# Performance work log

Hardware: AMD Instinct MI355X
Metric: run time of the kernel (lower is better)

The kernel has to match this reference:

```python
import jax, jax.numpy as jnp
import numpy as np

B, S, H, NH, HD = 2, 2048, 2048, 16, 128


def _bit_linear(x, w):
    """Ternary STE BitLinear: absmean scaling, round/clamp, fp matmul, rescale."""
    eps = 1e-5
    wn = w / (jnp.abs(w).mean() + eps)
    # straight-through estimator: forward uses quantized weights, grad flows to wn
    wq = wn + jax.lax.stop_gradient(jnp.clip(jnp.round(wn), -1.0, 1.0) - wn)
    y = x @ wq.T
    scale = w.shape[1]  # in_features
    Qb = 128.0  # 2**(8-1)
    return jnp.clip(y / scale * Qb, -Qb, Qb)


def _rotate_half(x):
    x1, x2 = jnp.split(x, 2, axis=-1)
    return jnp.concatenate([-x2, x1], axis=-1)


def setup_inputs() -> dict:
    key = jax.random.key(0)
    k1, k2, k3 = jax.random.split(key, 3)
    x = jax.random.normal(k1, (B, S, H), dtype=jnp.float32)
    w_qkv = jax.random.normal(k2, (3 * H, H), dtype=jnp.float32) * 0.02
    w_o = jax.random.normal(k3, (H, H), dtype=jnp.float32) * 0.02
    # realistic RoPE table [2, S, HD]
    inv_freq = 1.0 / (10000.0 ** (jnp.arange(0, HD, 2, dtype=jnp.float32) / HD))
    freqs = jnp.arange(S, dtype=jnp.float32)[:, None] * inv_freq[None, :]
    emb = jnp.concatenate([freqs, freqs], axis=-1)  # [S, HD]
    rotary = jnp.stack([jnp.cos(emb), jnp.sin(emb)], axis=0)
    return {"x": x, "rotary": rotary, "w_qkv": w_qkv, "w_o": w_o}


def reference(x, rotary, w_qkv, w_o):
    qkv = _bit_linear(x, w_qkv)  # [B, S, 3H]
    q, k, v = jnp.split(qkv, 3, axis=-1)
    q = q.reshape(B, S, NH, HD)
    k = k.reshape(B, S, NH, HD)
    v = v.reshape(B, S, NH, HD)
    cos = rotary[0][None, :, None, :]  # [1, S, 1, HD]
    sin = rotary[1][None, :, None, :]
    q = q * cos + _rotate_half(q) * sin
    k = k * cos + _rotate_half(k) * sin
    # [B, NH, S, HD]
    q, k, v = (t.transpose(0, 2, 1, 3) for t in (q, k, v))
    scores = jnp.einsum("bhqd,bhkd->bhqk", q, k) / np.sqrt(HD).astype(np.float32)
    causal = jnp.tril(jnp.ones((S, S), dtype=bool))
    scores = jnp.where(causal[None, None], scores, -jnp.inf)
    attn = jax.nn.softmax(scores, axis=-1)
    y = jnp.einsum("bhqk,bhkd->bhqd", attn, v)
    y = y.transpose(0, 2, 1, 3).reshape(B, S, H)
    return _bit_linear(y, w_o)
```

## Files before the change

### kernel.cpp

```cpp
#include <hip/hip_runtime.h>
#include <hip/hip_bf16.h>
#include <stdint.h>

#define B_   2
#define S_   2048
#define H_   2048
#define NH_  16
#define HD_  128
#define MTOK 4096
#define NQKV 6144

typedef unsigned short u16;
typedef __attribute__((ext_vector_type(8))) __bf16 bf16x8;
typedef __attribute__((ext_vector_type(4))) float f32x4;
typedef __attribute__((ext_vector_type(16))) float f32x16;

static __device__ __forceinline__ float bf2f(u16 u){
  union { uint32_t i; float f; } v; v.i = ((uint32_t)u) << 16; return v.f;
}
static __device__ __forceinline__ u16 f2bf(float f){
  union { float f; uint32_t i; } v; v.f = f;
  uint32_t r = v.i + 0x7FFFu + ((v.i >> 16) & 1u);
  return (u16)(r >> 16);
}
static __device__ __forceinline__ uint32_t cvt_pk_bf16(float lo, float hi){
  uint32_t r;
  asm("v_cvt_pk_bf16_f32 %0, %1, %2" : "=v"(r) : "v"(lo), "v"(hi));
  return r;
}
static __device__ __forceinline__ void pl32swap(uint32_t &a, uint32_t &b){
  asm volatile("v_permlane32_swap_b32 %0, %1" : "+v"(a), "+v"(b));
}

__device__ __forceinline__ void gload_lds16(const void* g, void* l){
  __builtin_amdgcn_global_load_lds((const __attribute__((address_space(1))) void*)g,
                                   (__attribute__((address_space(3))) void*)l, 16, 0, 0);
}

__global__ void absum_kernel(const float* __restrict__ w, int n, float* __restrict__ partial){
  __shared__ float sm[256];
  float s = 0.f;
  for (int i = blockIdx.x*256 + threadIdx.x; i < n; i += gridDim.x*256)
    s += fabsf(w[i]);
  sm[threadIdx.x] = s; __syncthreads();
  for (int st = 128; st > 0; st >>= 1){
    if ((int)threadIdx.x < st) sm[threadIdx.x] += sm[threadIdx.x + st];
    __syncthreads();
  }
  if (threadIdx.x == 0) partial[blockIdx.x] = sm[0];
}

__global__ void finalize_kernel(const float* __restrict__ p1, const float* __restrict__ p2,
                                float* __restrict__ scales){
  __shared__ double sm[256];
  int t = threadIdx.x;
  double s = (double)p1[t] + (double)p1[t+256] + (double)p1[t+512] + (double)p1[t+768];
  sm[t] = s; __syncthreads();
  for (int st = 128; st > 0; st >>= 1){ if (t < st) sm[t] += sm[t+st]; __syncthreads(); }
  if (t == 0) scales[0] = (float)(1.0 / (sm[0] / (double)(3*H_*H_) + 1e-5));
  __syncthreads();
  s = (double)p2[t] + (double)p2[t+256] + (double)p2[t+512] + (double)p2[t+768];
  sm[t] = s; __syncthreads();
  for (int st = 128; st > 0; st >>= 1){ if (t < st) sm[t] += sm[t+st]; __syncthreads(); }
  if (t == 0) scales[1] = (float)(1.0 / (sm[0] / (double)(H_*H_) + 1e-5));
}

__global__ void quant_kernel(const float* __restrict__ w, u16* __restrict__ wq, int n,
                             const float* __restrict__ scales, int which){
  float inv = scales[which];
  for (int i = blockIdx.x*256 + threadIdx.x; i < n; i += gridDim.x*256){
    float q = rintf(w[i] * inv);
    q = fminf(1.f, fmaxf(-1.f, q));
    wq[i] = f2bf(q);
  }
}

__global__ void castx_kernel(const float* __restrict__ x, u16* __restrict__ xb, int n){
  int i = blockIdx.x*256 + threadIdx.x;
  if (i < n) xb[i] = f2bf(x[i]);
}

template<int EPI>
__global__ __launch_bounds__(256) void gemm_kernel(const u16* __restrict__ A,
    const u16* __restrict__ Bw, int M, int N, int K,
    float* __restrict__ outf, u16* __restrict__ qb, u16* __restrict__ kb, u16* __restrict__ vtb)
{
  __shared__ u16 As[128*32];
  __shared__ u16 Bs[128*32];
  int nbn = N >> 7;
  int nb_tot = (M >> 7) * nbn;
  int bid = blockIdx.x;
  int chunk = nb_tot >> 3;
  bid = (bid & 7) * chunk + (bid >> 3);
  int bm = bid / nbn, bn = bid % nbn;
  int m0 = bm << 7, n0 = bn << 7;
  int tid = threadIdx.x;
  int lane = tid & 63, wid = tid >> 6;
  int wr = wid >> 1, wc = wid & 1;
  int lg = lane >> 4, lr = lane & 15;

  const u16* Ab = A + m0 * K;
  const u16* Bb = Bw + n0 * K;
  int srow = tid >> 2;
  int scol = (tid & 3) << 3;

  f32x4 acc[4][4];
  #pragma unroll
  for (int i = 0; i < 4; i++)
    #pragma unroll
    for (int j = 0; j < 4; j++) acc[i][j] = f32x4{0.f,0.f,0.f,0.f};

  for (int k0 = 0; k0 < K; k0 += 32){
    gload_lds16(Ab + srow*K      + k0 + scol, As + tid*8);
    gload_lds16(Ab + (srow+64)*K + k0 + scol, As + 2048 + tid*8);
    gload_lds16(Bb + srow*K      + k0 + scol, Bs + tid*8);
    gload_lds16(Bb + (srow+64)*K + k0 + scol, Bs + 2048 + tid*8);
    __syncthreads();
    bf16x8 af[4], bfr[4];
    #pragma unroll
    for (int mi = 0; mi < 4; mi++) af[mi]  = *(const bf16x8*)(As + ((wr*64 + mi*16 + lr)*32 + lg*8));
    #pragma unroll
    for (int ni = 0; ni < 4; ni++) bfr[ni] = *(const bf16x8*)(Bs + ((wc*64 + ni*16 + lr)*32 + lg*8));
    #pragma unroll
    for (int mi = 0; mi < 4; mi++)
      #pragma unroll
      for (int ni = 0; ni < 4; ni++)
        acc[mi][ni] = __builtin_amdgcn_mfma_f32_16x16x32_bf16(af[mi], bfr[ni], acc[mi][ni], 0, 0, 0);
    __syncthreads();
  }

  #pragma unroll
  for (int mi = 0; mi < 4; mi++){
    #pragma unroll
    for (int ni = 0; ni < 4; ni++){
      int ncol = n0 + wc*64 + ni*16 + lr;
      #pragma unroll
      for (int r = 0; r < 4; r++){
        int m = m0 + wr*64 + mi*16 + lg*4 + r;
        float v = acc[mi][ni][r] * 0.0625f;
        v = fminf(128.f, fmaxf(-128.f, v));
        if (EPI == 1){
          outf[m*N + ncol] = v;
        } else {
          int b = m >> 11, s = m & 2047;
          int part = ncol >> 11, c = ncol & 2047;
          int h = c >> 7, d = c & 127;
          int bh = b*NH_ + h;
          u16 bv = f2bf(v);
          if (part == 0)      qb[((bh*S_ + s) << 7) + d] = bv;
          else if (part == 1) kb[((bh*S_ + s) << 7) + d] = bv;
          else                vtb[((bh*HD_ + d) << 11) + s] = bv;
        }
      }
    }
  }
}

__global__ void rope_kernel(u16* __restrict__ qb, u16* __restrict__ kb, const float* __restrict__ rot){
  int i = blockIdx.x*256 + threadIdx.x;
  int d = i & 63;
  int s = (i >> 6) & 2047;
  int bh = (i >> 17) & 31;
  u16* buf = (i >> 22) ? kb : qb;
  int base = (bh*S_ + s)*HD_;
  float c  = rot[s*HD_ + d];
  float sn = rot[S_*HD_ + s*HD_ + d];
  float x1 = bf2f(buf[base + d]);
  float x2 = bf2f(buf[base + d + 64]);
  buf[base + d]      = f2bf(x1*c - x2*sn);
  buf[base + d + 64] = f2bf(x2*c + x1*sn);
}

__global__ __launch_bounds__(256) void attn_kernel(const u16* __restrict__ qb,
    const u16* __restrict__ kb, const u16* __restrict__ vtb, u16* __restrict__ ao)
{
  __shared__ alignas(16) u16 Ks[2][4096];
  __shared__ alignas(16) u16 Vs[2][4096];

  int bid = blockIdx.x;
  int sbid = (bid & 7)*64 + (bid >> 3);
  int bh = sbid >> 4;
  int bq = 15 - (sbid & 15);
  int tid = threadIdx.x;
  int wid = tid >> 6, lane = tid & 63;
  int l31 = lane & 31, hl = lane >> 5;
  int q0 = bq * 128;
  int qw = q0 + wid*32;
  int q  = qw + l31;

  const u16* Qp = qb + (size_t)(bh*S_ + qw)*HD_;
  const u16* Kp = kb + (size_t)bh*S_*HD_;
  const u16* Vt = vtb + (size_t)bh*HD_*S_;

  bf16x8 qf[8];
  #pragma unroll
  for (int t = 0; t < 8; t++)
    qf[t] = *(const bf16x8*)(Qp + l31*HD_ + t*16 + hl*8);

  f32x16 o[4];
  #pragma unroll
  for (int i = 0; i < 4; i++)
    #pragma unroll
    for (int j = 0; j < 16; j++) o[i][j] = 0.f;
  float m_r = -1e30f, l_r = 0.f;
  const float sm_scale = 0.08838834764831845f;

  auto STAGE = [&](int buf, int kt2){
    int t0 = wid*2;
    gload_lds16(Kp + (size_t)(kt2 + l31)*HD_ + (t0  )*16 + hl*8, &Ks[buf][((t0  )*64 + lane)*8]);
    gload_lds16(Kp + (size_t)(kt2 + l31)*HD_ + (t0+1)*16 + hl*8, &Ks[buf][((t0+1)*64 + lane)*8]);
    int v0 = wid*2, v1 = wid*2 + 1;
    gload_lds16(Vt + (size_t)((v0&3)*32 + l31)*S_ + kt2 + (v0>>2)*16 + hl*8, &Vs[buf][(v0*64 + lane)*8]);
    gload_lds16(Vt + (size_t)((v1&3)*32 + l31)*S_ + kt2 + (v1>>2)*16 + hl*8, &Vs[buf][(v1*64 + lane)*8]);
  };

  int n_it = 4*bq + 4;
  STAGE(0, 0);
  int cur = 0, kt = 0;
  for (int it = 0; it < n_it; ++it, kt += 32){
    if (it + 1 < n_it){
      STAGE(cur ^ 1, kt + 32);
      asm volatile("s_waitcnt vmcnt(4)" ::: "memory");
    } else {
      asm volatile("s_waitcnt vmcnt(0)" ::: "memory");
    }
    __builtin_amdgcn_sched_barrier(0);
    __builtin_amdgcn_s_barrier();

    if (kt <= qw){
      f32x16 sa;
      #pragma unroll
      for (int j = 0; j < 16; j++) sa[j] = 0.f;
      #pragma unroll
      for (int t = 0; t < 8; t++){
        bf16x8 kf = *(const bf16x8*)(&Ks[cur][(t*64 + lane)*8]);
        sa = __builtin_amdgcn_mfma_f32_32x32x16_bf16(kf, qf[t], sa, 0, 0, 0);
      }

      float sv[16];
      if (kt == qw){
        #pragma unroll
        for (int r = 0; r < 16; r++){
          int key = kt + (r&3) + 8*(r>>2) + 4*hl;
          sv[r] = (key > q) ? -1e30f : sa[r]*sm_scale;
        }
      } else {
        #pragma unroll
        for (int r = 0; r < 16; r++) sv[r] = sa[r]*sm_scale;
      }

      float pm = sv[0];
      #pragma unroll
      for (int r = 1; r < 16; r++) pm = fmaxf(pm, sv[r]);
      pm = fmaxf(pm, __shfl_xor(pm, 32));
      if (!__all(pm - m_r <= 8.f)){
        float mn = fmaxf(m_r, pm);
        float scl = __expf(m_r - mn);
        m_r = mn; l_r *= scl;
        #pragma unroll
        for (int i = 0; i < 4; i++)
          #pragma unroll
          for (int j = 0; j < 16; j++) o[i][j] *= scl;
      }
      float p[16];
      #pragma unroll
      for (int r = 0; r < 16; r++) p[r] = __expf(sv[r] - m_r);
      float ts = 0.f;
      #pragma unroll
      for (int r = 0; r < 16; r++) ts += p[r];
      ts += __shfl_xor(ts, 32);
      l_r += ts;

      uint32_t a0 = cvt_pk_bf16(p[0],  p[1]),  a1 = cvt_pk_bf16(p[2],  p[3]);
      uint32_t a2 = cvt_pk_bf16(p[4],  p[5]),  a3 = cvt_pk_bf16(p[6],  p[7]);
      uint32_t b0 = cvt_pk_bf16(p[8],  p[9]),  b1 = cvt_pk_bf16(p[10], p[11]);
      uint32_t b2 = cvt_pk_bf16(p[12], p[13]), b3 = cvt_pk_bf16(p[14], p[15]);
      pl32swap(a0, a2); pl32swap(a1, a3);
      pl32swap(b0, b2); pl32swap(b1, b3);
      union { uint32_t u[4]; bf16x8 v; } pf0, pf1;
      pf0.u[0]=a0; pf0.u[1]=a1; pf0.u[2]=a2; pf0.u[3]=a3;
      pf1.u[0]=b0; pf1.u[1]=b1; pf1.u[2]=b2; pf1.u[3]=b3;

      #pragma unroll
      for (int db = 0; db < 4; db++){
        bf16x8 vf0 = *(const bf16x8*)(&Vs[cur][((0*4 + db)*64 + lane)*8]);
        o[db] = __builtin_amdgcn_mfma_f32_32x32x16_bf16(vf0, pf0.v, o[db], 0, 0, 0);
        bf16x8 vf1 = *(const bf16x8*)(&Vs[cur][((1*4 + db)*64 + lane)*8]);
        o[db] = __builtin_amdgcn_mfma_f32_32x32x16_bf16(vf1, pf1.v, o[db], 0, 0, 0);
      }
      asm volatile("s_waitcnt lgkmcnt(0)" ::: "memory");
    }
    __builtin_amdgcn_sched_barrier(0);
    __builtin_amdgcn_s_barrier();
    cur ^= 1;
  }

  float inv = 1.f / l_r;
  int b = bh >> 4, hh = bh & 15;
  u16* orow = ao + (size_t)(b*S_ + q)*H_ + hh*HD_;
  #pragma unroll
  for (int db = 0; db < 4; db++){
    #pragma unroll
    for (int g = 0; g < 4; g++){
      ushort4 pk4;
      pk4.x = f2bf(o[db][4*g+0]*inv);
      pk4.y = f2bf(o[db][4*g+1]*inv);
      pk4.z = f2bf(o[db][4*g+2]*inv);
      pk4.w = f2bf(o[db][4*g+3]*inv);
      *(ushort4*)(orow + db*32 + g*8 + hl*4) = pk4;
    }
  }
}

extern "C" void kernel_launch(void* const* d_in, const int* in_sizes, int n_in,
                              void* d_out, int out_size, void* d_ws, size_t ws_size,
                              hipStream_t stream) {
  const float* x      = (const float*)d_in[0];
  const float* rotary = (const float*)d_in[1];
  const float* w_qkv  = (const float*)d_in[2];
  const float* w_o    = (const float*)d_in[3];
  float* out = (float*)d_out;

  char* wsb = (char*)d_ws;
  float* part_qkv = (float*)wsb;
  float* part_o   = part_qkv + 1024;
  float* scales   = part_o + 1024;
  size_t off = 16384;
  u16* xb    = (u16*)(wsb + off); off += (size_t)MTOK*H_*2;
  u16* wqkvq = (u16*)(wsb + off); off += (size_t)NQKV*H_*2;
  u16* woq   = (u16*)(wsb + off); off += (size_t)H_*H_*2;
  u16* qbuf  = (u16*)(wsb + off); off += (size_t)B_*NH_*S_*HD_*2;
  u16* kbuf  = (u16*)(wsb + off); off += (size_t)B_*NH_*S_*HD_*2;
  u16* vtb   = (u16*)(wsb + off); off += (size_t)B_*NH_*S_*HD_*2;
  u16* ao    = (u16*)(wsb + off); off += (size_t)MTOK*H_*2;

  absum_kernel<<<1024, 256, 0, stream>>>(w_qkv, 3*H_*H_, part_qkv);
  absum_kernel<<<1024, 256, 0, stream>>>(w_o, H_*H_, part_o);
  finalize_kernel<<<1, 256, 0, stream>>>(part_qkv, part_o, scales);
  quant_kernel<<<4096, 256, 0, stream>>>(w_qkv, wqkvq, 3*H_*H_, scales, 0);
  quant_kernel<<<2048, 256, 0, stream>>>(w_o, woq, H_*H_, scales, 1);
  castx_kernel<<<(MTOK*H_)/256, 256, 0, stream>>>(x, xb, MTOK*H_);

  gemm_kernel<0><<<(MTOK/128)*(NQKV/128), 256, 0, stream>>>(xb, wqkvq, MTOK, NQKV, H_,
                                                            nullptr, qbuf, kbuf, vtb);
  rope_kernel<<<(2*B_*NH_*S_*64)/256, 256, 0, stream>>>(qbuf, kbuf, rotary);
  attn_kernel<<<B_*NH_*(S_/128), 256, 0, stream>>>(qbuf, kbuf, vtb, ao);
  gemm_kernel<1><<<(MTOK/128)*(H_/128), 256, 0, stream>>>(ao, woq, MTOK, H_, H_,
                                                          out, nullptr, nullptr, nullptr);
}
```

Measured before the change: 400.5 us.

## Rework BitLinear GEMM into 128x256 tiles with triple-buffered async LDS pipeline

Both BitLinear GEMMs now use a 128x256 output tile with 512 threads (8 waves) and K-steps of 64. A 3-stage dynamic LDS ring is filled by direct global-to-LDS loads two iterations ahead. LDS is laid out in fragment-major order so each wave reads its MFMA operands contiguously. Waits use explicit vmcnt counts and raw s_barrier with raised wave priority around the MFMA block, which lets loads overlap compute and replaces the full syncthreads after every 32-wide K step. The cost is 144KB of LDS per block, which limits occupancy to one block per CU and makes correctness depend on hand-tuned wait counts.

```diff
diff --git a/kernel.cpp b/kernel.cpp
--- a/kernel.cpp
+++ b/kernel.cpp
@@ -81,28 +81,27 @@
 }
 
 template<int EPI>
-__global__ __launch_bounds__(256) void gemm_kernel(const u16* __restrict__ A,
+__global__ __launch_bounds__(512, 2) void gemm_kernel(const u16* __restrict__ A,
     const u16* __restrict__ Bw, int M, int N, int K,
     float* __restrict__ outf, u16* __restrict__ qb, u16* __restrict__ kb, u16* __restrict__ vtb)
 {
-  __shared__ u16 As[128*32];
-  __shared__ u16 Bs[128*32];
-  int nbn = N >> 7;
-  int nb_tot = (M >> 7) * nbn;
+  extern __shared__ u16 lds[];
+  int nbm = M >> 7;
+  int nb_tot = nbm * (N >> 8);
   int bid = blockIdx.x;
   int chunk = nb_tot >> 3;
-  bid = (bid & 7) * chunk + (bid >> 3);
-  int bm = bid / nbn, bn = bid % nbn;
-  int m0 = bm << 7, n0 = bn << 7;
+  int sb = (bid & 7)*chunk + (bid >> 3);
+  int bm = sb % nbm, bn = sb / nbm;
+  int m0 = bm << 7, n0 = bn << 8;
   int tid = threadIdx.x;
   int lane = tid & 63, wid = tid >> 6;
-  int wr = wid >> 1, wc = wid & 1;
-  int lg = lane >> 4, lr = lane & 15;
-
-  const u16* Ab = A + m0 * K;
-  const u16* Bb = Bw + n0 * K;
-  int srow = tid >> 2;
-  int scol = (tid & 3) << 3;
+  int wm = wid >> 2, wn = wid & 3;
+  int lr = lane & 15, lg = lane >> 4;
+  int lg8 = lg << 3;
+  int kw = (wid & 1) << 5;
+
+  const u16* Ab = A + (size_t)m0 * K;
+  const u16* Bb = Bw + (size_t)n0 * K;
 
   f32x4 acc[4][4];
   #pragma unroll
@@ -110,37 +109,70 @@
     #pragma unroll
     for (int j = 0; j < 4; j++) acc[i][j] = f32x4{0.f,0.f,0.f,0.f};
 
-  for (int k0 = 0; k0 < K; k0 += 32){
-    gload_lds16(Ab + srow*K      + k0 + scol, As + tid*8);
-    gload_lds16(Ab + (srow+64)*K + k0 + scol, As + 2048 + tid*8);
-    gload_lds16(Bb + srow*K      + k0 + scol, Bs + tid*8);
-    gload_lds16(Bb + (srow+64)*K + k0 + scol, Bs + 2048 + tid*8);
-    __syncthreads();
-    bf16x8 af[4], bfr[4];
-    #pragma unroll
-    for (int mi = 0; mi < 4; mi++) af[mi]  = *(const bf16x8*)(As + ((wr*64 + mi*16 + lr)*32 + lg*8));
-    #pragma unroll
-    for (int ni = 0; ni < 4; ni++) bfr[ni] = *(const bf16x8*)(Bs + ((wc*64 + ni*16 + lr)*32 + lg*8));
-    #pragma unroll
-    for (int mi = 0; mi < 4; mi++)
+  auto STAGE = [&](int tt, int vlo){
+    u16* ldst = lds + (tt % 3) * 24576;
+    int k0 = tt << 6;
+    #pragma unroll
+    for (int v = vlo; v < vlo + 3; v++){
+      int f = v*8 + wid;
+      const u16* src;
+      if (v < 2){
+        src = Ab + (size_t)(((f >> 1) << 4) + lr)*K + k0 + kw + lg8;
+      } else {
+        src = Bb + (size_t)((((f - 16) >> 1) << 4) + lr)*K + k0 + kw + lg8;
+      }
+      gload_lds16(src, ldst + f*512 + lane*8);
+    }
+  };
+
+  int NT = K >> 6;
+  STAGE(0,0); STAGE(0,3); STAGE(1,0); STAGE(1,3);
+  asm volatile("s_waitcnt vmcnt(6)" ::: "memory");
+  __builtin_amdgcn_sched_barrier(0);
+  __builtin_amdgcn_s_barrier();
+
+  for (int t = 0; t < NT; t++){
+    u16* bufp = lds + (t % 3) * 24576;
+    #pragma unroll
+    for (int ph = 0; ph < 2; ph++){
+      if (t + 2 < NT) STAGE(t + 2, ph*3);
+      bf16x8 af[4], bfr[4];
+      #pragma unroll
+      for (int mi = 0; mi < 4; mi++)
+        af[mi] = *(const bf16x8*)(bufp + (((wm*4 + mi)*2 + ph)*512) + lane*8);
       #pragma unroll
       for (int ni = 0; ni < 4; ni++)
-        acc[mi][ni] = __builtin_amdgcn_mfma_f32_16x16x32_bf16(af[mi], bfr[ni], acc[mi][ni], 0, 0, 0);
-    __syncthreads();
+        bfr[ni] = *(const bf16x8*)(bufp + ((16 + (wn*4 + ni)*2 + ph)*512) + lane*8);
+      __builtin_amdgcn_s_setprio(1);
+      #pragma unroll
+      for (int mi = 0; mi < 4; mi++)
+        #pragma unroll
+        for (int ni = 0; ni < 4; ni++)
+          acc[mi][ni] = __builtin_amdgcn_mfma_f32_16x16x32_bf16(af[mi], bfr[ni], acc[mi][ni], 0, 0, 0);
+      __builtin_amdgcn_s_setprio(0);
+      if (ph == 0){
+        __builtin_amdgcn_s_barrier();
+      } else {
+        if (t + 2 < NT) asm volatile("s_waitcnt vmcnt(6)" ::: "memory");
+        else            asm volatile("s_waitcnt vmcnt(0)" ::: "memory");
+        __builtin_amdgcn_sched_barrier(0);
+        __builtin_amdgcn_s_barrier();
+      }
+    }
   }
 
   #pragma unroll
   for (int mi = 0; mi < 4; mi++){
     #pragma unroll
     for (int ni = 0; ni < 4; ni++){
-      int ncol = n0 + wc*64 + ni*16 + lr;
+      int ncol = n0 + wn*64 + ni*16 + lr;
       #pragma unroll
       for (int r = 0; r < 4; r++){
-        int m = m0 + wr*64 + mi*16 + lg*4 + r;
+        int m = m0 + wm*64 + mi*16 + lg*4 + r;
         float v = acc[mi][ni][r] * 0.0625f;
         v = fminf(128.f, fmaxf(-128.f, v));
         if (EPI == 1){
-          outf[m*N + ncol] = v;
+          outf[(size_t)m*N + ncol] = v;
         } else {
           int b = m >> 11, s = m & 2047;
           int part = ncol >> 11, c = ncol & 2047;
@@ -334,6 +366,12 @@
   u16* vtb   = (u16*)(wsb + off); off += (size_t)B_*NH_*S_*HD_*2;
   u16* ao    = (u16*)(wsb + off); off += (size_t)MTOK*H_*2;
 
+  const int GEMM_LDS = 3 * 48 * 1024;
+  hipFuncSetAttribute((const void*)&gemm_kernel<0>,
+                      hipFuncAttributeMaxDynamicSharedMemorySize, GEMM_LDS);
+  hipFuncSetAttribute((const void*)&gemm_kernel<1>,
+                      hipFuncAttributeMaxDynamicSharedMemorySize, GEMM_LDS);
+
   absum_kernel<<<1024, 256, 0, stream>>>(w_qkv, 3*H_*H_, part_qkv);
   absum_kernel<<<1024, 256, 0, stream>>>(w_o, H_*H_, part_o);
   finalize_kernel<<<1, 256, 0, stream>>>(part_qkv, part_o, scales);
@@ -341,10 +379,10 @@
   quant_kernel<<<2048, 256, 0, stream>>>(w_o, woq, H_*H_, scales, 1);
   castx_kernel<<<(MTOK*H_)/256, 256, 0, stream>>>(x, xb, MTOK*H_);
 
-  gemm_kernel<0><<<(MTOK/128)*(NQKV/128), 256, 0, stream>>>(xb, wqkvq, MTOK, NQKV, H_,
-                                                            nullptr, qbuf, kbuf, vtb);
+  gemm_kernel<0><<<(MTOK/128)*(NQKV/256), 512, GEMM_LDS, stream>>>(xb, wqkvq, MTOK, NQKV, H_,
+                                                                   nullptr, qbuf, kbuf, vtb);
   rope_kernel<<<(2*B_*NH_*S_*64)/256, 256, 0, stream>>>(qbuf, kbuf, rotary);
   attn_kernel<<<B_*NH_*(S_/128), 256, 0, stream>>>(qbuf, kbuf, vtb, ao);
-  gemm_kernel<1><<<(MTOK/128)*(H_/128), 256, 0, stream>>>(ao, woq, MTOK, H_, H_,
-                                                          out, nullptr, nullptr, nullptr);
-}
+  gemm_kernel<1><<<(MTOK/128)*(H_/256), 512, GEMM_LDS, stream>>>(ao, woq, MTOK, H_, H_,
+                                                                 out, nullptr, nullptr, nullptr);
+}
```

New measurement: 421.4 us. 1.05x slower.

## Double-buffer GEMM LDS tiles with explicit vmcnt waits and fragment-major layout

Applied to the files above, without the earlier changes.

Rewrites the GEMM main loop to double-buffer the A and B LDS tiles, so the next K-slab's global-to-LDS loads are in flight while the current slab's MFMAs run. Explicit s_waitcnt vmcnt and raw barriers with sched_barrier replace __syncthreads. The LDS layout becomes fragment-contiguous (each 16x32 MFMA fragment stored as 64 lanes x 8 elements), making fragment reads conflict-free contiguous 16-byte loads. The block swizzle now walks M-major within chunks. This doubles LDS use, which could lower occupancy.

```diff
diff --git a/kernel.cpp b/kernel.cpp
--- a/kernel.cpp
+++ b/kernel.cpp
@@ -36,6 +36,11 @@
   __builtin_amdgcn_global_load_lds((const __attribute__((address_space(1))) void*)g,
                                    (__attribute__((address_space(3))) void*)l, 16, 0, 0);
 }
+
+#define BARR  __builtin_amdgcn_s_barrier()
+#define SCHB0 __builtin_amdgcn_sched_barrier(0)
+#define VMW4  do{ asm volatile("s_waitcnt vmcnt(4)" ::: "memory"); SCHB0; }while(0)
+#define VMW0  do{ asm volatile("s_waitcnt vmcnt(0)" ::: "memory"); SCHB0; }while(0)
 
 __global__ void absum_kernel(const float* __restrict__ w, int n, float* __restrict__ partial){
   __shared__ float sm[256];
@@ -85,24 +90,23 @@
     const u16* __restrict__ Bw, int M, int N, int K,
     float* __restrict__ outf, u16* __restrict__ qb, u16* __restrict__ kb, u16* __restrict__ vtb)
 {
-  __shared__ u16 As[128*32];
-  __shared__ u16 Bs[128*32];
-  int nbn = N >> 7;
-  int nb_tot = (M >> 7) * nbn;
+  __shared__ alignas(16) u16 As[2][4096];
+  __shared__ alignas(16) u16 Bs[2][4096];
+  int nbm = M >> 7;
+  int nb_tot = nbm * (N >> 7);
   int bid = blockIdx.x;
   int chunk = nb_tot >> 3;
-  bid = (bid & 7) * chunk + (bid >> 3);
-  int bm = bid / nbn, bn = bid % nbn;
+  int sb = (bid & 7)*chunk + (bid >> 3);
+  int bm = sb % nbm, bn = sb / nbm;
   int m0 = bm << 7, n0 = bn << 7;
   int tid = threadIdx.x;
   int lane = tid & 63, wid = tid >> 6;
   int wr = wid >> 1, wc = wid & 1;
-  int lg = lane >> 4, lr = lane & 15;
-
-  const u16* Ab = A + m0 * K;
-  const u16* Bb = Bw + n0 * K;
-  int srow = tid >> 2;
-  int scol = (tid & 3) << 3;
+  int lr = lane & 15, lg = lane >> 4;
+  int lg8 = lg << 3;
+
+  const u16* Ab = A + (size_t)m0 * K;
+  const u16* Bb = Bw + (size_t)n0 * K;
 
   f32x4 acc[4][4];
   #pragma unroll
@@ -110,23 +114,34 @@
     #pragma unroll
     for (int j = 0; j < 4; j++) acc[i][j] = f32x4{0.f,0.f,0.f,0.f};
 
-  for (int k0 = 0; k0 < K; k0 += 32){
-    gload_lds16(Ab + srow*K      + k0 + scol, As + tid*8);
-    gload_lds16(Ab + (srow+64)*K + k0 + scol, As + 2048 + tid*8);
-    gload_lds16(Bb + srow*K      + k0 + scol, Bs + tid*8);
-    gload_lds16(Bb + (srow+64)*K + k0 + scol, Bs + 2048 + tid*8);
-    __syncthreads();
+  auto STAGE = [&](int buf, int k0){
+    #pragma unroll
+    for (int j = 0; j < 2; j++){
+      int fa = wid*2 + j;
+      gload_lds16(Ab + (size_t)(fa*16 + lr)*K + k0 + lg8, &As[buf][fa*512 + lane*8]);
+      gload_lds16(Bb + (size_t)(fa*16 + lr)*K + k0 + lg8, &Bs[buf][fa*512 + lane*8]);
+    }
+  };
+
+  int NT = K >> 5;
+  STAGE(0, 0);
+  for (int t = 0; t < NT; t++){
+    int buf = t & 1;
+    if (t + 1 < NT){ STAGE(buf ^ 1, (t + 1) << 5); VMW4; }
+    else           { VMW0; }
+    BARR;
     bf16x8 af[4], bfr[4];
     #pragma unroll
-    for (int mi = 0; mi < 4; mi++) af[mi]  = *(const bf16x8*)(As + ((wr*64 + mi*16 + lr)*32 + lg*8));
-    #pragma unroll
-    for (int ni = 0; ni < 4; ni++) bfr[ni] = *(const bf16x8*)(Bs + ((wc*64 + ni*16 + lr)*32 + lg*8));
+    for (int mi = 0; mi < 4; mi++) af[mi]  = *(const bf16x8*)(&As[buf][(wr*4 + mi)*512 + lane*8]);
+    #pragma unroll
+    for (int ni = 0; ni < 4; ni++) bfr[ni] = *(const bf16x8*)(&Bs[buf][(wc*4 + ni)*512 + lane*8]);
     #pragma unroll
     for (int mi = 0; mi < 4; mi++)
       #pragma unroll
       for (int ni = 0; ni < 4; ni++)
         acc[mi][ni] = __builtin_amdgcn_mfma_f32_16x16x32_bf16(af[mi], bfr[ni], acc[mi][ni], 0, 0, 0);
-    __syncthreads();
+    SCHB0;
+    BARR;
   }
 
   #pragma unroll
@@ -140,7 +155,7 @@
         float v = acc[mi][ni][r] * 0.0625f;
         v = fminf(128.f, fmaxf(-128.f, v));
         if (EPI == 1){
-          outf[m*N + ncol] = v;
+          outf[(size_t)m*N + ncol] = v;
         } else {
           int b = m >> 11, s = m & 2047;
           int part = ncol >> 11, c = ncol & 2047;
```

New measurement: 477.7 us. 19.3% more time.
